# Performance work log

Hardware: AMD Instinct MI355X
Metric: run time of the kernel (lower is better)

## Reference

```python
import jax, jax.numpy as jnp
import numpy as np
from jax import lax

EPS = 1e-6
MATCH_THRESHOLD = 0.3
N_DISCRETE_STEPS = 5
DT = 0.01
TWO_PI = 2.0 * np.pi


def setup_inputs() -> dict:
    key = jax.random.key(0)
    ks = jax.random.split(key, 6)
    N, M, D, H, n_osc = 8192, 8192, 4, 64, 28
    detections_t = jax.random.normal(ks[0], (N, D), dtype=jnp.float32)
    detections_t1 = jax.random.normal(ks[1], (M, D), dtype=jnp.float32)
    phase_W1 = jax.random.normal(ks[2], (D, H), dtype=jnp.float32) * (1.0 / np.sqrt(D))
    phase_b1 = jax.random.normal(ks[3], (H,), dtype=jnp.float32) * 0.05
    phase_W2 = jax.random.normal(ks[4], (H, n_osc), dtype=jnp.float32) * (1.0 / np.sqrt(H))
    phase_b2 = jax.random.normal(ks[5], (n_osc,), dtype=jnp.float32) * 0.05
    # fixed oscillator frequencies buffer: [2]*4 + [6]*8 + [40]*16
    frequencies = jnp.concatenate([
        jnp.full((4,), 2.0, jnp.float32),
        jnp.full((8,), 6.0, jnp.float32),
        jnp.full((16,), 40.0, jnp.float32),
    ])
    return {
        'detections_t': detections_t,
        'detections_t1': detections_t1,
        'phase_W1': phase_W1,
        'phase_b1': phase_b1,
        'phase_W2': phase_W2,
        'phase_b2': phase_b2,
        'frequencies': frequencies,
    }


def _encode_phase(x, W1, b1, W2, b2):
    h = jax.nn.relu(x @ W1 + b1)
    raw = h @ W2 + b2
    return raw % TWO_PI  # [N, n_osc]


def _similarity(phase_a, phase_b):
    # real(sum_k e^{i a_k} e^{-i b_k}) = cos(a)@cos(b).T + sin(a)@sin(b).T
    ca, sa = jnp.cos(phase_a), jnp.sin(phase_a)
    cb, sb = jnp.cos(phase_b), jnp.sin(phase_b)
    na = jnp.sqrt(jnp.sum(ca * ca + sa * sa, axis=-1, keepdims=True)) + EPS  # [N,1]
    nb = jnp.sqrt(jnp.sum(cb * cb + sb * sb, axis=-1, keepdims=True)) + EPS  # [M,1]
    sim = (ca @ cb.T + sa @ sb.T) / (na * nb.T)  # [N, M]
    return sim


def reference(detections_t, detections_t1, phase_W1, phase_b1, phase_W2, phase_b2, frequencies):
    phase_t = _encode_phase(detections_t, phase_W1, phase_b1, phase_W2, phase_b2)
    phase_t1 = _encode_phase(detections_t1, phase_W1, phase_b1, phase_W2, phase_b2)

    # uncoupled phase advance (n_discrete_steps fixed small loop)
    phase = phase_t
    for _ in range(N_DISCRETE_STEPS):
        phase = (phase + TWO_PI * frequencies * DT) % TWO_PI

    sim = _similarity(phase, phase_t1)  # [N, M]

    N = detections_t.shape[0]
    M = detections_t1.shape[0]
    max_sims = jnp.max(sim, axis=1)
    max_idxs = jnp.argmax(sim, axis=1)
    order = jnp.argsort(-max_sims)  # descending

    def body(i, carry):
        matches, used = carry
        idx = order[i]
        j = max_idxs[idx]
        ok = jnp.logical_and(jnp.logical_not(used[j]), max_sims[idx] > MATCH_THRESHOLD)
        matches = matches.at[idx].set(jnp.where(ok, j, -1))
        used = used.at[j].set(jnp.logical_or(used[j], ok))
        return (matches, used)

    matches0 = jnp.full((N,), -1, dtype=jnp.int32)
    used0 = jnp.zeros((M,), dtype=bool)
    matches, _ = lax.fori_loop(0, N, body, (matches0, used0))
    return (matches, sim)
```

## Files before the change

### kernel.cpp

```cpp
#include <hip/hip_runtime.h>
#include <math.h>

#define NR 8192
#define N_OSC 28
#define TWO_PI_F 6.28318530717958647692f
#define PLANE 524288

typedef __attribute__((ext_vector_type(8))) short s16x8;
typedef __attribute__((ext_vector_type(16))) float f32x16;
typedef __attribute__((ext_vector_type(4))) float f32x4;

#define AS3(p) ((__attribute__((address_space(3))) void*)(p))
#define AS1C(p) ((const __attribute__((address_space(1))) void*)(p))

__device__ __forceinline__ float modpos(float x) {
    float r = fmodf(x, TWO_PI_F);
    if (r < 0.0f) r += TWO_PI_F;
    return r;
}
__device__ __forceinline__ unsigned fmono(float f) {
    unsigned u = __float_as_uint(f);
    return (u & 0x80000000u) ? ~u : (u | 0x80000000u);
}
__device__ __forceinline__ unsigned short f2bf(float f) {
    unsigned u = __float_as_uint(f);
    return (unsigned short)((u + 0x7FFFu + ((u >> 16) & 1u)) >> 16);
}
__device__ __forceinline__ float bf2f(unsigned short h) {
    return __uint_as_float(((unsigned)h) << 16);
}

__global__ __launch_bounds__(64) void encode_kernel(
    const float* __restrict__ detA, const float* __restrict__ detB,
    const float* __restrict__ W1, const float* __restrict__ b1,
    const float* __restrict__ W2, const float* __restrict__ b2,
    const float* __restrict__ freq,
    unsigned short* __restrict__ tabA, unsigned short* __restrict__ tabB,
    float* __restrict__ normA, float* __restrict__ normB,
    unsigned long long* __restrict__ rowMax, unsigned long long* __restrict__ colWin)
{
    __shared__ float sW1[4 * 64];
    __shared__ float sb1[64];
    __shared__ float sW2[64 * N_OSC];
    __shared__ float sb2[N_OSC];
    __shared__ float sDelta[N_OSC];

    int t = threadIdx.x;
    for (int i = t; i < 4 * 64; i += 64) sW1[i] = W1[i];
    sb1[t] = b1[t];
    for (int i = t; i < 64 * N_OSC; i += 64) sW2[i] = W2[i];
    if (t < N_OSC) {
        sb2[t] = b2[t];
        sDelta[t] = (TWO_PI_F * freq[t]) * 0.01f;
    }
    __syncthreads();

    int gid = blockIdx.x * 64 + t;
    bool isA = gid < NR;
    int row = isA ? gid : gid - NR;
    const float* det = isA ? detA : detB;
    unsigned short* tab = isA ? tabA : tabB;
    float* nrm = isA ? normA : normB;

    if (isA) rowMax[gid] = 0ull; else colWin[gid - NR] = 0ull;

    float4 xv = *(const float4*)(det + (size_t)row * 4);
    float x0 = xv.x, x1 = xv.y, x2 = xv.z, x3 = xv.w;

    float h[64];
#pragma unroll
    for (int j = 0; j < 64; ++j) {
        float a = x0 * sW1[0 * 64 + j];
        a += x1 * sW1[1 * 64 + j];
        a += x2 * sW1[2 * 64 + j];
        a += x3 * sW1[3 * 64 + j];
        a += sb1[j];
        h[j] = fmaxf(a, 0.0f);
    }

    float raw[N_OSC];
#pragma unroll
    for (int o = 0; o < N_OSC; ++o) raw[o] = 0.0f;
#pragma unroll
    for (int j = 0; j < 64; ++j) {
        float hj = h[j];
#pragma unroll
        for (int o = 0; o < N_OSC; ++o) raw[o] += hj * sW2[j * N_OSC + o];
    }

    int rs = row & 7;
    size_t rbase = (size_t)row * 64;
    float csum = 0.0f;
#pragma unroll
    for (int o = 0; o < N_OSC; ++o) {
        float p = raw[o] + sb2[o];
        p = modpos(p);
        if (isA) {
            float d = sDelta[o];
#pragma unroll
            for (int s = 0; s < 5; ++s) { p = modpos(p + d); }
        }
        float sn, cs;
        sincosf(p, &sn, &cs);
        csum += cs * cs + sn * sn;
        {
            int k = o;
            unsigned short h0 = f2bf(cs); float r1 = cs - bf2f(h0);
            unsigned short h1 = f2bf(r1); float r2 = r1 - bf2f(h1);
            unsigned short h2 = f2bf(r2);
            size_t e = rbase + ((((k >> 3) ^ rs) << 3) | (k & 7));
            tab[e] = h0; tab[PLANE + e] = h1; tab[2 * PLANE + e] = h2;
        }
        {
            int k = 28 + o;
            unsigned short h0 = f2bf(sn); float r1 = sn - bf2f(h0);
            unsigned short h1 = f2bf(r1); float r2 = r1 - bf2f(h1);
            unsigned short h2 = f2bf(r2);
            size_t e = rbase + ((((k >> 3) ^ rs) << 3) | (k & 7));
            tab[e] = h0; tab[PLANE + e] = h1; tab[2 * PLANE + e] = h2;
        }
    }
#pragma unroll
    for (int k = 56; k < 64; ++k) {
        size_t e = rbase + ((((k >> 3) ^ rs) << 3) | (k & 7));
        tab[e] = 0; tab[PLANE + e] = 0; tab[2 * PLANE + e] = 0;
    }
    nrm[row] = 1.0f / (sqrtf(csum) + 1e-6f);
}

__device__ __forceinline__ void stage_plane(const unsigned short* __restrict__ tab,
                                            int dim0, unsigned short* dst,
                                            int w, int l)
{
#pragma unroll
    for (int i = 0; i < 4; ++i) {
        int u = w * 4 + i;
        const unsigned short* g = tab + (size_t)(dim0 + 8 * u + (l >> 3)) * 64 + (l & 7) * 8;
        __builtin_amdgcn_global_load_lds(AS1C(g), AS3(dst + u * 512), 16, 0, 0);
    }
}

__global__ __launch_bounds__(256) void sim_kernel(
    const unsigned short* __restrict__ tabA, const unsigned short* __restrict__ tabB,
    const float* __restrict__ normA, const float* __restrict__ normB,
    float* __restrict__ simOut, unsigned long long* __restrict__ rowMax)
{
    __shared__ __align__(16) unsigned char smem[81920];
    unsigned short* Bsh0 = (unsigned short*)(smem);
    unsigned short* Bsh1 = (unsigned short*)(smem + 16384);
    unsigned short* Bsh2 = (unsigned short*)(smem + 32768);
    unsigned short* Ash0 = (unsigned short*)(smem + 49152);
    unsigned short* Ash1 = (unsigned short*)(smem + 65536);

    int bid = blockIdx.x;
    int swz = (bid & 7) * 512 + (bid >> 3);
    int bx = swz & 63, by = swz >> 6;
    int r0 = by * 128, c0 = bx * 128;

    int t = threadIdx.x, w = t >> 6, l = t & 63;
    int wr = w >> 1, wc = w & 1;
    int lrow = l & 31;
    int kh2 = (l >> 5) * 16;
    int sw = (lrow & 7) << 4;

    stage_plane(tabB, c0, Bsh0, w, l);
    stage_plane(tabB + PLANE, c0, Bsh1, w, l);
    stage_plane(tabB + 2 * PLANE, c0, Bsh2, w, l);
    stage_plane(tabA, r0, Ash0, w, l);
    __syncthreads();
    stage_plane(tabA + PLANE, r0, Ash1, w, l);

    f32x16 acc00, acc01, acc10, acc11;
#pragma unroll
    for (int r = 0; r < 16; ++r) { acc00[r] = 0.f; acc01[r] = 0.f; acc10[r] = 0.f; acc11[r] = 0.f; }

    int baA0 = (wr * 64 + lrow) * 128, baA1 = baA0 + 32 * 128;
    int baB0 = (wc * 64 + lrow) * 128, baB1 = baB0 + 32 * 128;

#define FR(arr, ba, ks) (*(const s16x8*)((const char*)(arr) + (ba) + (((ks) * 32 + kh2) ^ sw)))

    s16x8 bh0[4], bh1[4];
    s16x8 bm0[4], bm1[4];

#pragma unroll
    for (int ks = 0; ks < 4; ++ks) {
        s16x8 a0 = FR(Ash0, baA0, ks), a1 = FR(Ash0, baA1, ks);
        bh0[ks] = FR(Bsh0, baB0, ks); bh1[ks] = FR(Bsh0, baB1, ks);
        acc00 = __builtin_amdgcn_mfma_f32_32x32x16_bf16(a0, bh0[ks], acc00, 0, 0, 0);
        acc01 = __builtin_amdgcn_mfma_f32_32x32x16_bf16(a0, bh1[ks], acc01, 0, 0, 0);
        acc10 = __builtin_amdgcn_mfma_f32_32x32x16_bf16(a1, bh0[ks], acc10, 0, 0, 0);
        acc11 = __builtin_amdgcn_mfma_f32_32x32x16_bf16(a1, bh1[ks], acc11, 0, 0, 0);
        bm0[ks] = FR(Bsh1, baB0, ks); bm1[ks] = FR(Bsh1, baB1, ks);
        acc00 = __builtin_amdgcn_mfma_f32_32x32x16_bf16(a0, bm0[ks], acc00, 0, 0, 0);
        acc01 = __builtin_amdgcn_mfma_f32_32x32x16_bf16(a0, bm1[ks], acc01, 0, 0, 0);
        acc10 = __builtin_amdgcn_mfma_f32_32x32x16_bf16(a1, bm0[ks], acc10, 0, 0, 0);
        acc11 = __builtin_amdgcn_mfma_f32_32x32x16_bf16(a1, bm1[ks], acc11, 0, 0, 0);
        s16x8 b0 = FR(Bsh2, baB0, ks), b1 = FR(Bsh2, baB1, ks);
        acc00 = __builtin_amdgcn_mfma_f32_32x32x16_bf16(a0, b0, acc00, 0, 0, 0);
        acc01 = __builtin_amdgcn_mfma_f32_32x32x16_bf16(a0, b1, acc01, 0, 0, 0);
        acc10 = __builtin_amdgcn_mfma_f32_32x32x16_bf16(a1, b0, acc10, 0, 0, 0);
        acc11 = __builtin_amdgcn_mfma_f32_32x32x16_bf16(a1, b1, acc11, 0, 0, 0);
    }
    __syncthreads();
    stage_plane(tabA + 2 * PLANE, r0, Ash0, w, l);

#pragma unroll
    for (int ks = 0; ks < 4; ++ks) {
        s16x8 a0 = FR(Ash1, baA0, ks), a1 = FR(Ash1, baA1, ks);
        acc00 = __builtin_amdgcn_mfma_f32_32x32x16_bf16(a0, bh0[ks], acc00, 0, 0, 0);
        acc01 = __builtin_amdgcn_mfma_f32_32x32x16_bf16(a0, bh1[ks], acc01, 0, 0, 0);
        acc10 = __builtin_amdgcn_mfma_f32_32x32x16_bf16(a1, bh0[ks], acc10, 0, 0, 0);
        acc11 = __builtin_amdgcn_mfma_f32_32x32x16_bf16(a1, bh1[ks], acc11, 0, 0, 0);
        acc00 = __builtin_amdgcn_mfma_f32_32x32x16_bf16(a0, bm0[ks], acc00, 0, 0, 0);
        acc01 = __builtin_amdgcn_mfma_f32_32x32x16_bf16(a0, bm1[ks], acc01, 0, 0, 0);
        acc10 = __builtin_amdgcn_mfma_f32_32x32x16_bf16(a1, bm0[ks], acc10, 0, 0, 0);
        acc11 = __builtin_amdgcn_mfma_f32_32x32x16_bf16(a1, bm1[ks], acc11, 0, 0, 0);
    }
    __syncthreads();

#pragma unroll
    for (int ks = 0; ks < 4; ++ks) {
        s16x8 a0 = FR(Ash0, baA0, ks), a1 = FR(Ash0, baA1, ks);
        acc00 = __builtin_amdgcn_mfma_f32_32x32x16_bf16(a0, bh0[ks], acc00, 0, 0, 0);
        acc01 = __builtin_amdgcn_mfma_f32_32x32x16_bf16(a0, bh1[ks], acc01, 0, 0, 0);
        acc10 = __builtin_amdgcn_mfma_f32_32x32x16_bf16(a1, bh0[ks], acc10, 0, 0, 0);
        acc11 = __builtin_amdgcn_mfma_f32_32x32x16_bf16(a1, bh1[ks], acc11, 0, 0, 0);
    }
#undef FR

    float icn0 = normB[c0 + wc * 64 + lrow];
    float icn1 = normB[c0 + wc * 64 + 32 + lrow];

    __syncthreads();
    float* scr = (float*)(smem + w * 17408);

#pragma unroll
    for (int r = 0; r < 16; ++r) {
        int rd0 = (r & 3) + 8 * (r >> 2) + 4 * (l >> 5);
        float irn0 = normA[r0 + wr * 64 + rd0];
        scr[rd0 * 68 + lrow]      = acc00[r] * (irn0 * icn0);
        scr[rd0 * 68 + 32 + lrow] = acc01[r] * (irn0 * icn1);
        int rd1 = rd0 + 32;
        float irn1 = normA[r0 + wr * 64 + rd1];
        scr[rd1 * 68 + lrow]      = acc10[r] * (irn1 * icn0);
        scr[rd1 * 68 + 32 + lrow] = acc11[r] * (irn1 * icn1);
    }

#pragma unroll
    for (int s = 0; s < 16; ++s) {
        int lr = 4 * s + (l >> 4);
        f32x4 v = *(const f32x4*)&scr[lr * 68 + (l & 15) * 4];
        int grow = r0 + wr * 64 + lr;
        __builtin_nontemporal_store(v,
            (f32x4*)&simOut[(size_t)grow * NR + c0 + wc * 64 + (l & 15) * 4]);
    }

    {
        const float* rp = &scr[l * 68];
        float mv = -2.0f; int mc = 0;
#pragma unroll
        for (int c4 = 0; c4 < 16; ++c4) {
            f32x4 v = *(const f32x4*)&rp[c4 * 4];
#pragma unroll
            for (int e = 0; e < 4; ++e) {
                bool g = v[e] > mv;
                mv = g ? v[e] : mv;
                mc = g ? c4 * 4 + e : mc;
            }
        }
        int grow = r0 + wr * 64 + l;
        unsigned gcol = (unsigned)(c0 + wc * 64 + mc);
        unsigned long long key = ((unsigned long long)fmono(mv) << 32)
                               | (unsigned long long)(0xFFFFFFFFu - gcol);
        atomicMax(&rowMax[grow], key);
    }
}

__global__ __launch_bounds__(256) void rowwin_kernel(
    const unsigned long long* __restrict__ rowMax,
    unsigned long long* __restrict__ colWin,
    float* __restrict__ outMatches)
{
    int r = blockIdx.x * 256 + threadIdx.x;
    if (r >= NR) return;
    outMatches[r] = -1.0f;
    unsigned long long key = rowMax[r];
    unsigned m = (unsigned)(key >> 32);
    unsigned bits = (m & 0x80000000u) ? (m ^ 0x80000000u) : ~m;
    float ms = __uint_as_float(bits);
    unsigned col = 0xFFFFFFFFu - (unsigned)key;
    if (ms > 0.3f) {
        unsigned long long ck = ((unsigned long long)m << 32)
                              | (unsigned long long)(0xFFFFFFFFu - (unsigned)r);
        atomicMax(&colWin[col], ck);
    }
}

__global__ __launch_bounds__(256) void colfin_kernel(
    const unsigned long long* __restrict__ colWin,
    float* __restrict__ outMatches)
{
    int j = blockIdx.x * 256 + threadIdx.x;
    if (j >= NR) return;
    unsigned long long w = colWin[j];
    if (w != 0ull) {
        unsigned r = 0xFFFFFFFFu - (unsigned)w;
        outMatches[r] = (float)j;
    }
}

extern "C" void kernel_launch(void* const* d_in, const int* in_sizes, int n_in,
                              void* d_out, int out_size, void* d_ws, size_t ws_size,
                              hipStream_t stream) {
    const float* detA = (const float*)d_in[0];
    const float* detB = (const float*)d_in[1];
    const float* W1   = (const float*)d_in[2];
    const float* b1   = (const float*)d_in[3];
    const float* W2   = (const float*)d_in[4];
    const float* b2   = (const float*)d_in[5];
    const float* freq = (const float*)d_in[6];
    float* out = (float*)d_out;

    char* ws = (char*)d_ws;
    unsigned short* tabA = (unsigned short*)(ws);
    unsigned short* tabB = (unsigned short*)(ws + 3145728);
    float* normA = (float*)(ws + 6291456);
    float* normB = (float*)(ws + 6324224);
    unsigned long long* rowMax = (unsigned long long*)(ws + 6356992);
    unsigned long long* colWin = (unsigned long long*)(ws + 6422528);

    encode_kernel<<<256, 64, 0, stream>>>(detA, detB, W1, b1, W2, b2, freq,
                                          tabA, tabB, normA, normB, rowMax, colWin);
    sim_kernel<<<4096, 256, 0, stream>>>(tabA, tabB, normA, normB, out + NR, rowMax);
    rowwin_kernel<<<NR / 256, 256, 0, stream>>>(rowMax, colWin, out);
    colfin_kernel<<<NR / 256, 256, 0, stream>>>(colWin, out);
}
```

Measured before the change: 127.8 us.

## Enlarge sim tile to 256x128 with 512 threads and stage all planes at once

The similarity kernel now uses 256-row by 128-column tiles with 8 waves per block, halving the grid. All three bf16 split planes of A and B are loaded into shared memory in one pass before a single barrier, replacing the staged, double-synchronized plane loading. The goal is fewer barriers and more reuse of the B tile per block. The cost is 144KB of LDS per block, which limits occupancy to one block per CU and removes overlap between loads and MFMA work. The epilogue still indexes scratch as w*17408 for 8 waves, so it may overrun the LDS allocation or stay unchanged incorrectly.

Measured after the change: 126.9 us. Within noise of the previous version (-0.7%).

```diff
diff --git a/kernel.cpp b/kernel.cpp
--- a/kernel.cpp
+++ b/kernel.cpp
@@ -128,34 +128,17 @@
     nrm[row] = 1.0f / (sqrtf(csum) + 1e-6f);
 }
 
-__device__ __forceinline__ void stage_plane(const unsigned short* __restrict__ tab,
-                                            int dim0, unsigned short* dst,
-                                            int w, int l)
-{
-#pragma unroll
-    for (int i = 0; i < 4; ++i) {
-        int u = w * 4 + i;
-        const unsigned short* g = tab + (size_t)(dim0 + 8 * u + (l >> 3)) * 64 + (l & 7) * 8;
-        __builtin_amdgcn_global_load_lds(AS1C(g), AS3(dst + u * 512), 16, 0, 0);
-    }
-}
-
-__global__ __launch_bounds__(256) void sim_kernel(
+__global__ __launch_bounds__(512) void sim_kernel(
     const unsigned short* __restrict__ tabA, const unsigned short* __restrict__ tabB,
     const float* __restrict__ normA, const float* __restrict__ normB,
     float* __restrict__ simOut, unsigned long long* __restrict__ rowMax)
 {
-    __shared__ __align__(16) unsigned char smem[81920];
-    unsigned short* Bsh0 = (unsigned short*)(smem);
-    unsigned short* Bsh1 = (unsigned short*)(smem + 16384);
-    unsigned short* Bsh2 = (unsigned short*)(smem + 32768);
-    unsigned short* Ash0 = (unsigned short*)(smem + 49152);
-    unsigned short* Ash1 = (unsigned short*)(smem + 65536);
+    __shared__ __align__(16) unsigned char smem[147456];
 
     int bid = blockIdx.x;
-    int swz = (bid & 7) * 512 + (bid >> 3);
+    int swz = (bid & 7) * 256 + (bid >> 3);
     int bx = swz & 63, by = swz >> 6;
-    int r0 = by * 128, c0 = bx * 128;
+    int r0 = by * 256, c0 = bx * 128;
 
     int t = threadIdx.x, w = t >> 6, l = t & 63;
     int wr = w >> 1, wc = w & 1;
@@ -163,70 +146,67 @@
     int kh2 = (l >> 5) * 16;
     int sw = (lrow & 7) << 4;
 
-    stage_plane(tabB, c0, Bsh0, w, l);
-    stage_plane(tabB + PLANE, c0, Bsh1, w, l);
-    stage_plane(tabB + 2 * PLANE, c0, Bsh2, w, l);
-    stage_plane(tabA, r0, Ash0, w, l);
+#pragma unroll
+    for (int i = 0; i < 18; ++i) {
+        int u = w * 18 + i;
+        const unsigned short* src;
+        if (u < 48) {
+            int p = u >> 4, rem = u & 15;
+            src = tabB + (size_t)p * PLANE + (size_t)(c0 + rem * 8 + (l >> 3)) * 64 + (l & 7) * 8;
+        } else {
+            int v = u - 48;
+            int p = v >> 5, rem = v & 31;
+            src = tabA + (size_t)p * PLANE + (size_t)(r0 + rem * 8 + (l >> 3)) * 64 + (l & 7) * 8;
+        }
+        __builtin_amdgcn_global_load_lds(AS1C(src), AS3(smem + u * 1024), 16, 0, 0);
+    }
     __syncthreads();
-    stage_plane(tabA + PLANE, r0, Ash1, w, l);
 
     f32x16 acc00, acc01, acc10, acc11;
 #pragma unroll
     for (int r = 0; r < 16; ++r) { acc00[r] = 0.f; acc01[r] = 0.f; acc10[r] = 0.f; acc11[r] = 0.f; }
 
-    int baA0 = (wr * 64 + lrow) * 128, baA1 = baA0 + 32 * 128;
-    int baB0 = (wc * 64 + lrow) * 128, baB1 = baB0 + 32 * 128;
-
-#define FR(arr, ba, ks) (*(const s16x8*)((const char*)(arr) + (ba) + (((ks) * 32 + kh2) ^ sw)))
-
-    s16x8 bh0[4], bh1[4];
-    s16x8 bm0[4], bm1[4];
+    int baA = (wr * 64 + lrow) * 128;
+    int baB = (wc * 64 + lrow) * 128;
+
+#define FRB(p, ba, ks) (*(const s16x8*)(smem + (p) * 16384 + (ba) + (((ks) * 32 + kh2) ^ sw)))
+#define FRA(p, ba, ks) (*(const s16x8*)(smem + 49152 + (p) * 32768 + (ba) + (((ks) * 32 + kh2) ^ sw)))
 
 #pragma unroll
     for (int ks = 0; ks < 4; ++ks) {
-        s16x8 a0 = FR(Ash0, baA0, ks), a1 = FR(Ash0, baA1, ks);
-        bh0[ks] = FR(Bsh0, baB0, ks); bh1[ks] = FR(Bsh0, baB1, ks);
-        acc00 = __builtin_amdgcn_mfma_f32_32x32x16_bf16(a0, bh0[ks], acc00, 0, 0, 0);
-        acc01 = __builtin_amdgcn_mfma_f32_32x32x16_bf16(a0, bh1[ks], acc01, 0, 0, 0);
-        acc10 = __builtin_amdgcn_mfma_f32_32x32x16_bf16(a1, bh0[ks], acc10, 0, 0, 0);
-        acc11 = __builtin_amdgcn_mfma_f32_32x32x16_bf16(a1, bh1[ks], acc11, 0, 0, 0);
-        bm0[ks] = FR(Bsh1, baB0, ks); bm1[ks] = FR(Bsh1, baB1, ks);
-        acc00 = __builtin_amdgcn_mfma_f32_32x32x16_bf16(a0, bm0[ks], acc00, 0, 0, 0);
-        acc01 = __builtin_amdgcn_mfma_f32_32x32x16_bf16(a0, bm1[ks], acc01, 0, 0, 0);
-        acc10 = __builtin_amdgcn_mfma_f32_32x32x16_bf16(a1, bm0[ks], acc10, 0, 0, 0);
-        acc11 = __builtin_amdgcn_mfma_f32_32x32x16_bf16(a1, bm1[ks], acc11, 0, 0, 0);
-        s16x8 b0 = FR(Bsh2, baB0, ks), b1 = FR(Bsh2, baB1, ks);
-        acc00 = __builtin_amdgcn_mfma_f32_32x32x16_bf16(a0, b0, acc00, 0, 0, 0);
-        acc01 = __builtin_amdgcn_mfma_f32_32x32x16_bf16(a0, b1, acc01, 0, 0, 0);
-        acc10 = __builtin_amdgcn_mfma_f32_32x32x16_bf16(a1, b0, acc10, 0, 0, 0);
-        acc11 = __builtin_amdgcn_mfma_f32_32x32x16_bf16(a1, b1, acc11, 0, 0, 0);
-    }
-    __syncthreads();
-    stage_plane(tabA + 2 * PLANE, r0, Ash0, w, l);
-
-#pragma unroll
-    for (int ks = 0; ks < 4; ++ks) {
-        s16x8 a0 = FR(Ash1, baA0, ks), a1 = FR(Ash1, baA1, ks);
-        acc00 = __builtin_amdgcn_mfma_f32_32x32x16_bf16(a0, bh0[ks], acc00, 0, 0, 0);
-        acc01 = __builtin_amdgcn_mfma_f32_32x32x16_bf16(a0, bh1[ks], acc01, 0, 0, 0);
-        acc10 = __builtin_amdgcn_mfma_f32_32x32x16_bf16(a1, bh0[ks], acc10, 0, 0, 0);
-        acc11 = __builtin_amdgcn_mfma_f32_32x32x16_bf16(a1, bh1[ks], acc11, 0, 0, 0);
-        acc00 = __builtin_amdgcn_mfma_f32_32x32x16_bf16(a0, bm0[ks], acc00, 0, 0, 0);
-        acc01 = __builtin_amdgcn_mfma_f32_32x32x16_bf16(a0, bm1[ks], acc01, 0, 0, 0);
-        acc10 = __builtin_amdgcn_mfma_f32_32x32x16_bf16(a1, bm0[ks], acc10, 0, 0, 0);
-        acc11 = __builtin_amdgcn_mfma_f32_32x32x16_bf16(a1, bm1[ks], acc11, 0, 0, 0);
-    }
-    __syncthreads();
-
-#pragma unroll
-    for (int ks = 0; ks < 4; ++ks) {
-        s16x8 a0 = FR(Ash0, baA0, ks), a1 = FR(Ash0, baA1, ks);
-        acc00 = __builtin_amdgcn_mfma_f32_32x32x16_bf16(a0, bh0[ks], acc00, 0, 0, 0);
-        acc01 = __builtin_amdgcn_mfma_f32_32x32x16_bf16(a0, bh1[ks], acc01, 0, 0, 0);
-        acc10 = __builtin_amdgcn_mfma_f32_32x32x16_bf16(a1, bh0[ks], acc10, 0, 0, 0);
-        acc11 = __builtin_amdgcn_mfma_f32_32x32x16_bf16(a1, bh1[ks], acc11, 0, 0, 0);
-    }
-#undef FR
+        s16x8 ah0 = FRA(0, baA, ks),            ah1 = FRA(0, baA + 4096, ks);
+        s16x8 bh0 = FRB(0, baB, ks),            bh1 = FRB(0, baB + 4096, ks);
+        acc00 = __builtin_amdgcn_mfma_f32_32x32x16_bf16(ah0, bh0, acc00, 0, 0, 0);
+        acc01 = __builtin_amdgcn_mfma_f32_32x32x16_bf16(ah0, bh1, acc01, 0, 0, 0);
+        acc10 = __builtin_amdgcn_mfma_f32_32x32x16_bf16(ah1, bh0, acc10, 0, 0, 0);
+        acc11 = __builtin_amdgcn_mfma_f32_32x32x16_bf16(ah1, bh1, acc11, 0, 0, 0);
+        s16x8 bm0 = FRB(1, baB, ks),            bm1 = FRB(1, baB + 4096, ks);
+        acc00 = __builtin_amdgcn_mfma_f32_32x32x16_bf16(ah0, bm0, acc00, 0, 0, 0);
+        acc01 = __builtin_amdgcn_mfma_f32_32x32x16_bf16(ah0, bm1, acc01, 0, 0, 0);
+        acc10 = __builtin_amdgcn_mfma_f32_32x32x16_bf16(ah1, bm0, acc10, 0, 0, 0);
+        acc11 = __builtin_amdgcn_mfma_f32_32x32x16_bf16(ah1, bm1, acc11, 0, 0, 0);
+        s16x8 bl0 = FRB(2, baB, ks),            bl1 = FRB(2, baB + 4096, ks);
+        acc00 = __builtin_amdgcn_mfma_f32_32x32x16_bf16(ah0, bl0, acc00, 0, 0, 0);
+        acc01 = __builtin_amdgcn_mfma_f32_32x32x16_bf16(ah0, bl1, acc01, 0, 0, 0);
+        acc10 = __builtin_amdgcn_mfma_f32_32x32x16_bf16(ah1, bl0, acc10, 0, 0, 0);
+        acc11 = __builtin_amdgcn_mfma_f32_32x32x16_bf16(ah1, bl1, acc11, 0, 0, 0);
+        s16x8 am0 = FRA(1, baA, ks),            am1 = FRA(1, baA + 4096, ks);
+        acc00 = __builtin_amdgcn_mfma_f32_32x32x16_bf16(am0, bh0, acc00, 0, 0, 0);
+        acc01 = __builtin_amdgcn_mfma_f32_32x32x16_bf16(am0, bh1, acc01, 0, 0, 0);
+        acc10 = __builtin_amdgcn_mfma_f32_32x32x16_bf16(am1, bh0, acc10, 0, 0, 0);
+        acc11 = __builtin_amdgcn_mfma_f32_32x32x16_bf16(am1, bh1, acc11, 0, 0, 0);
+        acc00 = __builtin_amdgcn_mfma_f32_32x32x16_bf16(am0, bm0, acc00, 0, 0, 0);
+        acc01 = __builtin_amdgcn_mfma_f32_32x32x16_bf16(am0, bm1, acc01, 0, 0, 0);
+        acc10 = __builtin_amdgcn_mfma_f32_32x32x16_bf16(am1, bm0, acc10, 0, 0, 0);
+        acc11 = __builtin_amdgcn_mfma_f32_32x32x16_bf16(am1, bm1, acc11, 0, 0, 0);
+        s16x8 al0 = FRA(2, baA, ks),            al1 = FRA(2, baA + 4096, ks);
+        acc00 = __builtin_amdgcn_mfma_f32_32x32x16_bf16(al0, bh0, acc00, 0, 0, 0);
+        acc01 = __builtin_amdgcn_mfma_f32_32x32x16_bf16(al0, bh1, acc01, 0, 0, 0);
+        acc10 = __builtin_amdgcn_mfma_f32_32x32x16_bf16(al1, bh0, acc10, 0, 0, 0);
+        acc11 = __builtin_amdgcn_mfma_f32_32x32x16_bf16(al1, bh1, acc11, 0, 0, 0);
+    }
+#undef FRA
+#undef FRB
 
     float icn0 = normB[c0 + wc * 64 + lrow];
     float icn1 = normB[c0 + wc * 64 + 32 + lrow];
@@ -331,7 +311,7 @@
 
     encode_kernel<<<256, 64, 0, stream>>>(detA, detB, W1, b1, W2, b2, freq,
                                           tabA, tabB, normA, normB, rowMax, colWin);
-    sim_kernel<<<4096, 256, 0, stream>>>(tabA, tabB, normA, normB, out + NR, rowMax);
+    sim_kernel<<<2048, 512, 0, stream>>>(tabA, tabB, normA, normB, out + NR, rowMax);
     rowwin_kernel<<<NR / 256, 256, 0, stream>>>(rowMax, colWin, out);
     colfin_kernel<<<NR / 256, 256, 0, stream>>>(colWin, out);
 }
```
